# Kernel optimization log

Measured on AMD Instinct MI355X. Metric: run time of the kernel, lower is better.

## Reference

```python
import jax, jax.numpy as jnp
import numpy as np

N = 100000      # nodes
E = 1600000     # edges (avg degree 16)
F_IN = 128      # num_features
H = 64          # num_hidden
C = 40          # num_classes


def setup_inputs() -> dict:
    key = jax.random.key(0)
    ks = jax.random.split(key, 12)
    glorot = lambda k, fi, fo: jax.random.normal(k, (fi, fo), jnp.float32) * np.float32(1.0 / np.sqrt(fi))
    return {
        "x": jax.random.normal(ks[0], (N, F_IN), jnp.float32),
        "edge_index": jax.random.randint(ks[1], (2, E), 0, N, jnp.int64),
        "conv0_w": glorot(ks[2], F_IN, H), "conv0_b": jnp.zeros((H,), jnp.float32),
        "lin0_w": glorot(ks[3], H, H),     "lin0_b": jnp.zeros((H,), jnp.float32),
        "conv1_w": glorot(ks[4], H, H),    "conv1_b": jnp.zeros((H,), jnp.float32),
        "lin1_w": glorot(ks[5], H, H),     "lin1_b": jnp.zeros((H,), jnp.float32),
        "out_w": glorot(ks[6], 2 * H, C),  "out_b": jnp.zeros((C,), jnp.float32),
    }


def _gcn_conv(h, W, b, src, dst, norm, n):
    # h: [N, din] -> transform then symmetric-normalized scatter-add aggregation
    m = (h @ W)[src] * norm[:, None]           # [E+N, dout] gathered messages
    return jax.ops.segment_sum(m, dst, num_segments=n) + b


def reference(x, edge_index, conv0_w, conv0_b, lin0_w, lin0_b,
              conv1_w, conv1_b, lin1_w, lin1_b, out_w, out_b):
    n = x.shape[0]
    loops = jnp.arange(n, dtype=edge_index.dtype)
    src = jnp.concatenate([edge_index[0], loops])  # self-loops appended (GCNConv default)
    dst = jnp.concatenate([edge_index[1], loops])
    deg = jax.ops.segment_sum(jnp.ones_like(dst, x.dtype), dst, num_segments=n)
    dinv = jnp.where(deg > 0, jax.lax.rsqrt(deg), 0.0)
    norm = dinv[src] * dinv[dst]                   # D^-1/2 A D^-1/2 edge weights

    # layer 0 (dropout omitted: eval mode for deterministic reference)
    h = jax.nn.elu(_gcn_conv(x, conv0_w, conv0_b, src, dst, norm, n))
    y0 = h @ lin0_w + lin0_b
    # layer 1
    h = jax.nn.elu(_gcn_conv(h, conv1_w, conv1_b, src, dst, norm, n))
    y1 = h @ lin1_w + lin1_b

    z = jnp.concatenate([y0, y1], axis=1)          # [N, 2H] jumping-knowledge concat
    return z @ out_w + out_b                       # [N, C]
```

## Files before the change

### kernel.cpp

```cpp
#include <hip/hip_runtime.h>

#define DEVFN __device__ __forceinline__

typedef __attribute__((ext_vector_type(8))) short short8;
typedef __attribute__((ext_vector_type(4))) float float4v;

DEVFN float bf2f(unsigned short u) {
    union { unsigned int i; float f; } c;
    c.i = ((unsigned int)u) << 16;
    return c.f;
}

DEVFN unsigned short f2bf(float f) {
    union { float f; unsigned int i; } c;
    c.f = f;
    unsigned int u = c.i;
    return (unsigned short)((u + 0x7FFFu + ((u >> 16) & 1u)) >> 16);
}

DEVFN void addu4(float* acc, uint4 u) {
    unsigned int w[4] = {u.x, u.y, u.z, u.w};
#pragma unroll
    for (int k = 0; k < 4; k++) {
        union { unsigned int i; float f; } lo, hi;
        lo.i = w[k] << 16;
        hi.i = w[k] & 0xFFFF0000u;
        acc[2 * k]     += lo.f;
        acc[2 * k + 1] += hi.f;
    }
}


#define CHUNK 4096

__global__ __launch_bounds__(256) void k_count(const int* __restrict__ dst,
                                               int* __restrict__ Cmat, int E) {
    __shared__ int lh[1024];
    int t = threadIdx.x;
    for (int b = t; b < 1024; b += 256) lh[b] = 0;
    __syncthreads();
    int i0 = blockIdx.x * CHUNK;
    int i1 = i0 + CHUNK; if (i1 > E) i1 = E;
    for (int i = i0 + t; i < i1; i += 256) atomicAdd(&lh[dst[i] >> 8], 1);
    __syncthreads();
    int* row = Cmat + (size_t)blockIdx.x * 1024;
    for (int b = t; b < 1024; b += 256) row[b] = lh[b];
}

__global__ __launch_bounds__(256) void k_wscan(const int* __restrict__ Cmat,
                                               int* __restrict__ Omat,
                                               int* __restrict__ btot, int gC) {
    int b = (blockIdx.x * 256 + threadIdx.x) >> 6;
    int lane = threadIdx.x & 63;
    int base = 0;
    for (int c0 = 0; c0 < gC; c0 += 64) {
        int c = c0 + lane;
        int x = (c < gC) ? Cmat[(size_t)c * 1024 + b] : 0;
        int orig = x;
#pragma unroll
        for (int off = 1; off < 64; off <<= 1) {
            int y = __shfl_up(x, off);
            if (lane >= off) x += y;
        }
        if (c < gC) Omat[(size_t)c * 1024 + b] = base + x - orig;
        base += __shfl(x, 63);
    }
    if (lane == 0) btot[b] = base;
}

__global__ __launch_bounds__(1024) void k_bscan(const int* __restrict__ btot,
                                                int* __restrict__ boff) {
    __shared__ int s[1024];
    int t = threadIdx.x;
    int v = btot[t];
    s[t] = v;
    __syncthreads();
    for (int o = 1; o < 1024; o <<= 1) {
        int x = (t >= o) ? s[t - o] : 0;
        __syncthreads();
        s[t] += x;
        __syncthreads();
    }
    boff[t] = s[t] - v;
    if (t == 1023) boff[1024] = s[t];
}

__global__ __launch_bounds__(256) void k_part2(const int* __restrict__ src,
                                               const int* __restrict__ dst,
                                               const int* __restrict__ Omat,
                                               const int* __restrict__ boff,
                                               unsigned int* __restrict__ part, int E) {
    __shared__ int lb[1024];
    __shared__ int lc[1024];
    int t = threadIdx.x;
    const int* orow = Omat + (size_t)blockIdx.x * 1024;
    for (int b = t; b < 1024; b += 256) {
        lb[b] = boff[b] + orow[b];
        lc[b] = 0;
    }
    __syncthreads();
    int i0 = blockIdx.x * CHUNK;
    int i1 = i0 + CHUNK; if (i1 > E) i1 = E;
    for (int i = i0 + t; i < i1; i += 256) {
        int d = dst[i];
        int b = d >> 8;
        int r = atomicAdd(&lc[b], 1);
        part[lb[b] + r] = (unsigned int)src[i] | ((unsigned int)(d & 255) << 24);
    }
}

__global__ __launch_bounds__(256) void k_fill_local(const unsigned int* __restrict__ part,
                                                    const int* __restrict__ boff,
                                                    float* __restrict__ dinv,
                                                    int* __restrict__ roff,
                                                    int* __restrict__ csr, int n) {
    __shared__ int lcnt[256];
    __shared__ int lsc[256];
    __shared__ int lcur[256];
    int b = blockIdx.x, t = threadIdx.x;
    int s0 = boff[b], s1 = boff[b + 1];
    lcnt[t] = 0;
    __syncthreads();
    for (int i = s0 + t; i < s1; i += 256) atomicAdd(&lcnt[part[i] >> 24], 1);
    __syncthreads();
    int v = lcnt[t];
    lsc[t] = v;
    __syncthreads();
    for (int o = 1; o < 256; o <<= 1) {
        int x = (t >= o) ? lsc[t - o] : 0;
        __syncthreads();
        lsc[t] += x;
        __syncthreads();
    }
    int excl = lsc[t] - v;
    int node = (b << 8) + t;
    if (node < n) {
        dinv[node] = rsqrtf((float)(v + 1));
        roff[node] = s0 + excl + v;
    }
    lcur[t] = s0 + excl;
    __syncthreads();
    for (int i = s0 + t; i < s1; i += 256) {
        unsigned int p = part[i];
        int pos = atomicAdd(&lcur[p >> 24], 1);
        csr[pos] = (int)(p & 0xFFFFFFu);
    }
}

__global__ __launch_bounds__(256) void k_prep(const float* __restrict__ W0,
                                              const float* __restrict__ W1,
                                              const float* __restrict__ lin0_w, const float* __restrict__ lin0_b,
                                              const float* __restrict__ lin1_w, const float* __restrict__ lin1_b,
                                              const float* __restrict__ out_w, const float* __restrict__ out_b,
                                              unsigned short* __restrict__ Wb0,
                                              unsigned short* __restrict__ Wb1,
                                              unsigned short* __restrict__ Wfb0,
                                              float* __restrict__ Wf1p,
                                              float* __restrict__ bfv) {
    int tid = blockIdx.x * 256 + threadIdx.x;
    if (tid < 1024) {
        int ks = tid >> 8, rem = tid & 255;
        int nt = rem >> 6, lane = rem & 63;
        int quad = lane >> 4, c = lane & 15;
        union { unsigned short h[8]; uint4 u; } p;
#pragma unroll
        for (int j = 0; j < 8; j++)
            p.h[j] = f2bf(W0[(ks * 32 + quad * 8 + j) * 64 + nt * 16 + c]);
        *(uint4*)(Wb0 + (size_t)tid * 8) = p.u;
    } else if (tid < 1536) {
        int t2 = tid - 1024;
        int ks = t2 >> 8, rem = t2 & 255;
        int nt = rem >> 6, lane = rem & 63;
        int quad = lane >> 4, c = lane & 15;
        union { unsigned short h[8]; uint4 u; } p;
#pragma unroll
        for (int j = 0; j < 8; j++)
            p.h[j] = f2bf(W1[(ks * 32 + quad * 8 + j) * 64 + nt * 16 + c]);
        *(uint4*)(Wb1 + (size_t)t2 * 8) = p.u;
    } else if (tid < 1920) {
        int t2 = tid - 1536;
        int ks = t2 / 192;
        int rem = t2 % 192;
        int nt = rem >> 6, lane = rem & 63;
        int quad = lane >> 4, c = lane & 15;
        int col = nt * 16 + c;
        union { unsigned short h[8]; uint4 u; } p;
#pragma unroll
        for (int j = 0; j < 8; j++) {
            unsigned short r = 0;
            if (col < 40) {
                int i = ks * 32 + quad * 8 + j;
                float a = 0.f;
                for (int k = 0; k < 64; k++) a += lin0_w[i * 64 + k] * out_w[k * 40 + col];
                r = f2bf(a);
            }
            p.h[j] = r;
        }
        *(uint4*)(Wfb0 + ((size_t)(ks * 3 + nt) * 64 + lane) * 8) = p.u;
    } else if (tid < 1960) {
        int j = tid - 1920;
        float a = out_b[j];
        for (int k = 0; k < 64; k++) {
            a += lin0_b[k] * out_w[k * 40 + j];
            a += lin1_b[k] * out_w[(64 + k) * 40 + j];
        }
        bfv[j] = a;
    } else if (tid < 4520) {
        int t2 = tid - 1960;
        int i = t2 / 40, c = t2 % 40;
        float a = 0.f;
        for (int k = 0; k < 64; k++) a += lin1_w[i * 64 + k] * out_w[(64 + k) * 40 + c];
        Wf1p[i * 40 + c] = a;
    }
}


__global__ __launch_bounds__(256) void k_gemm_128(const float* __restrict__ A,
                                                  const unsigned short* __restrict__ Wb,
                                                  const float* __restrict__ dinv,
                                                  unsigned short* __restrict__ Cb, int n) {
    __shared__ unsigned short aLDS[64 * 144];
    int t = threadIdx.x;
    int r0 = blockIdx.x * 64;
    for (int idx = t; idx < 2048; idx += 256) {
        int r = idx >> 5;
        int k = (idx & 31) << 2;
        int gr = r0 + r; if (gr >= n) gr = n - 1;
        float4 u = *(const float4*)(A + (size_t)gr * 128 + k);
        int tile = r >> 4, m = r & 15;
        int ks = k >> 5, quad = (k >> 3) & 3, j0 = k & 7;
        int g = (tile * 4 + ks) * 4 + quad;
        union { unsigned short h[4]; uint2 u2; } pk;
        pk.h[0] = f2bf(u.x); pk.h[1] = f2bf(u.y); pk.h[2] = f2bf(u.z); pk.h[3] = f2bf(u.w);
        *(uint2*)(aLDS + g * 144 + m * 8 + j0) = pk.u2;
    }
    int lane = t & 63;
    int w = t >> 6;
    short8 bfr[4][4];
#pragma unroll
    for (int ks = 0; ks < 4; ks++)
#pragma unroll
        for (int nt = 0; nt < 4; nt++)
            bfr[ks][nt] = *(const short8*)(Wb + ((size_t)(ks * 4 + nt) * 64 + lane) * 8);
    __syncthreads();
    int quad = lane >> 4, m = lane & 15;
    short8 afr[4];
#pragma unroll
    for (int ks = 0; ks < 4; ks++)
        afr[ks] = *(const short8*)(aLDS + ((w * 4 + ks) * 4 + quad) * 144 + m * 8);
    float4v acc[4] = {};
#pragma unroll
    for (int nt = 0; nt < 4; nt++)
#pragma unroll
        for (int ks = 0; ks < 4; ks++)
            acc[nt] = __builtin_amdgcn_mfma_f32_16x16x32_bf16(afr[ks], bfr[ks][nt], acc[nt], 0, 0, 0);
    float dv[4];
#pragma unroll
    for (int reg = 0; reg < 4; reg++) {
        int gr = r0 + w * 16 + quad * 4 + reg;
        dv[reg] = (gr < n) ? dinv[gr] : 0.f;
    }
#pragma unroll
    for (int nt = 0; nt < 4; nt++)
#pragma unroll
        for (int reg = 0; reg < 4; reg++) {
            int gr = r0 + w * 16 + quad * 4 + reg;
            if (gr < n) Cb[(size_t)gr * 64 + nt * 16 + m] = f2bf(dv[reg] * acc[nt][reg]);
        }
}

__global__ __launch_bounds__(256) void k_mid(const unsigned short* __restrict__ Hb,
                                             const unsigned short* __restrict__ Wb,
                                             const unsigned short* __restrict__ Wfb,
                                             const float* __restrict__ dinv,
                                             unsigned short* __restrict__ Ab,
                                             float* __restrict__ O, int n) {
    __shared__ unsigned short aLDS[32 * 144];
    int t = threadIdx.x;
    int r0 = blockIdx.x * 64;
    for (int idx = t; idx < 512; idx += 256) {
        int r = idx >> 3, j = idx & 7;
        int gr = r0 + r; if (gr >= n) gr = n - 1;
        uint4 u = *(const uint4*)(Hb + (size_t)gr * 64 + j * 8);
        int tile = r >> 4, m = r & 15;
        int ks = j >> 2, quad = j & 3;
        *(uint4*)(aLDS + ((tile * 2 + ks) * 4 + quad) * 144 + m * 8) = u;
    }
    int lane = t & 63;
    int w = t >> 6;
    short8 bG[2][4], bH[2][3];
#pragma unroll
    for (int ks = 0; ks < 2; ks++) {
#pragma unroll
        for (int nt = 0; nt < 4; nt++)
            bG[ks][nt] = *(const short8*)(Wb + ((size_t)(ks * 4 + nt) * 64 + lane) * 8);
#pragma unroll
        for (int nt = 0; nt < 3; nt++)
            bH[ks][nt] = *(const short8*)(Wfb + ((size_t)(ks * 3 + nt) * 64 + lane) * 8);
    }
    __syncthreads();
    int quad = lane >> 4, m = lane & 15;
    short8 afr[2];
#pragma unroll
    for (int ks = 0; ks < 2; ks++)
        afr[ks] = *(const short8*)(aLDS + ((w * 2 + ks) * 4 + quad) * 144 + m * 8);
    float4v accG[4] = {};
    float4v accH[3] = {};
#pragma unroll
    for (int nt = 0; nt < 4; nt++)
#pragma unroll
        for (int ks = 0; ks < 2; ks++)
            accG[nt] = __builtin_amdgcn_mfma_f32_16x16x32_bf16(afr[ks], bG[ks][nt], accG[nt], 0, 0, 0);
#pragma unroll
    for (int nt = 0; nt < 3; nt++)
#pragma unroll
        for (int ks = 0; ks < 2; ks++)
            accH[nt] = __builtin_amdgcn_mfma_f32_16x16x32_bf16(afr[ks], bH[ks][nt], accH[nt], 0, 0, 0);
    float dv[4];
#pragma unroll
    for (int reg = 0; reg < 4; reg++) {
        int gr = r0 + w * 16 + quad * 4 + reg;
        dv[reg] = (gr < n) ? dinv[gr] : 0.f;
    }
#pragma unroll
    for (int nt = 0; nt < 4; nt++)
#pragma unroll
        for (int reg = 0; reg < 4; reg++) {
            int gr = r0 + w * 16 + quad * 4 + reg;
            if (gr < n) Ab[(size_t)gr * 64 + nt * 16 + m] = f2bf(dv[reg] * accG[nt][reg]);
        }
#pragma unroll
    for (int nt = 0; nt < 3; nt++) {
        int col = nt * 16 + m;
        if (col < 40) {
#pragma unroll
            for (int reg = 0; reg < 4; reg++) {
                int gr = r0 + w * 16 + quad * 4 + reg;
                if (gr < n) O[(size_t)gr * 40 + col] = accH[nt][reg];
            }
        }
    }
}

__global__ __launch_bounds__(256) void k_agg(const unsigned short* __restrict__ T,
                                             const int* __restrict__ csr,
                                             const int* __restrict__ roffE,
                                             const float* __restrict__ bias,
                                             unsigned short* __restrict__ Hb, int n) {
    int lane = threadIdx.x & 63;
    int half = lane >> 5;
    int sub = lane & 31;
    int q = sub >> 3, h = sub & 7;
    int hb = half << 5;
    int v = blockIdx.x * 8 + ((threadIdx.x >> 6) << 1) + half;
    if (v >= n) return;
    int start = (v == 0) ? 0 : roffE[v - 1];
    int end = roffE[v];
    float dv = rsqrtf((float)(end - start + 1));
    float acc[8] = {0.f, 0.f, 0.f, 0.f, 0.f, 0.f, 0.f, 0.f};
    if (q == 0) {
        uint4 u = *(const uint4*)(T + (size_t)v * 64 + h * 8);
        addu4(acc, u);
    }
    for (int base = start; base < end; base += 32) {
        int m = end - base; if (m > 32) m = 32;
        int e = (sub < m) ? csr[base + sub] : 0;
        int j = 0;
        for (; j + 16 <= m; j += 16) {
            int s0 = __shfl(e, hb + j + q);
            int s1 = __shfl(e, hb + j + 4 + q);
            int s2 = __shfl(e, hb + j + 8 + q);
            int s3 = __shfl(e, hb + j + 12 + q);
            uint4 u0 = *(const uint4*)(T + (size_t)s0 * 64 + h * 8);
            uint4 u1 = *(const uint4*)(T + (size_t)s1 * 64 + h * 8);
            uint4 u2 = *(const uint4*)(T + (size_t)s2 * 64 + h * 8);
            uint4 u3 = *(const uint4*)(T + (size_t)s3 * 64 + h * 8);
            addu4(acc, u0); addu4(acc, u1); addu4(acc, u2); addu4(acc, u3);
        }
        if (j + 8 <= m) {
            int s0 = __shfl(e, hb + j + q);
            int s1 = __shfl(e, hb + j + 4 + q);
            uint4 u0 = *(const uint4*)(T + (size_t)s0 * 64 + h * 8);
            uint4 u1 = *(const uint4*)(T + (size_t)s1 * 64 + h * 8);
            addu4(acc, u0); addu4(acc, u1);
            j += 8;
        }
        if (j + 4 <= m) {
            int s = __shfl(e, hb + j + q);
            uint4 u = *(const uint4*)(T + (size_t)s * 64 + h * 8);
            addu4(acc, u);
            j += 4;
        }
        if (j < m) {
            int jj = j + q;
            int s = __shfl(e, hb + (jj & 31));
            if (jj < m) {
                uint4 u = *(const uint4*)(T + (size_t)s * 64 + h * 8);
                addu4(acc, u);
            }
        }
    }
#pragma unroll
    for (int i = 0; i < 8; i++) {
        acc[i] += __shfl_xor(acc[i], 8);
        acc[i] += __shfl_xor(acc[i], 16);
    }
    if (q == 0) {
        float4 b0 = *(const float4*)(bias + h * 8);
        float4 b1 = *(const float4*)(bias + h * 8 + 4);
        float bb[8] = {b0.x, b0.y, b0.z, b0.w, b1.x, b1.y, b1.z, b1.w};
        union { unsigned short hh[8]; uint4 u; } p;
#pragma unroll
        for (int i = 0; i < 8; i++) {
            float r = dv * acc[i] + bb[i];
            r = (r > 0.f) ? r : (__expf(r) - 1.f);
            p.hh[i] = f2bf(r);
        }
        *(uint4*)(Hb + (size_t)v * 64 + h * 8) = p.u;
    }
}

__global__ __launch_bounds__(256) void k_agg_head(const unsigned short* __restrict__ T,
                                                  const int* __restrict__ csr,
                                                  const int* __restrict__ roffE,
                                                  const float* __restrict__ bias,
                                                  const float* __restrict__ Wf1p,
                                                  const float* __restrict__ bfv,
                                                  float* __restrict__ O, int n) {
    __shared__ float Ws[64 * 41];
    int t = threadIdx.x;
    for (int idx = t; idx < 2560; idx += 256) {
        int k = idx / 40, c = idx % 40;
        Ws[k * 41 + c] = Wf1p[idx];
    }
    __syncthreads();
    int lane = t & 63;
    int half = lane >> 5;
    int sub = lane & 31;
    int q = sub >> 3, h = sub & 7;
    int hb = half << 5;
    int v = blockIdx.x * 8 + ((t >> 6) << 1) + half;
    if (v >= n) return;
    int start = (v == 0) ? 0 : roffE[v - 1];
    int end = roffE[v];
    float dv = rsqrtf((float)(end - start + 1));
    float acc[8] = {0.f, 0.f, 0.f, 0.f, 0.f, 0.f, 0.f, 0.f};
    if (q == 0) {
        uint4 u = *(const uint4*)(T + (size_t)v * 64 + h * 8);
        addu4(acc, u);
    }
    for (int base = start; base < end; base += 32) {
        int m = end - base; if (m > 32) m = 32;
        int e = (sub < m) ? csr[base + sub] : 0;
        int j = 0;
        for (; j + 16 <= m; j += 16) {
            int s0 = __shfl(e, hb + j + q);
            int s1 = __shfl(e, hb + j + 4 + q);
            int s2 = __shfl(e, hb + j + 8 + q);
            int s3 = __shfl(e, hb + j + 12 + q);
            uint4 u0 = *(const uint4*)(T + (size_t)s0 * 64 + h * 8);
            uint4 u1 = *(const uint4*)(T + (size_t)s1 * 64 + h * 8);
            uint4 u2 = *(const uint4*)(T + (size_t)s2 * 64 + h * 8);
            uint4 u3 = *(const uint4*)(T + (size_t)s3 * 64 + h * 8);
            addu4(acc, u0); addu4(acc, u1); addu4(acc, u2); addu4(acc, u3);
        }
        if (j + 8 <= m) {
            int s0 = __shfl(e, hb + j + q);
            int s1 = __shfl(e, hb + j + 4 + q);
            uint4 u0 = *(const uint4*)(T + (size_t)s0 * 64 + h * 8);
            uint4 u1 = *(const uint4*)(T + (size_t)s1 * 64 + h * 8);
            addu4(acc, u0); addu4(acc, u1);
            j += 8;
        }
        if (j + 4 <= m) {
            int s = __shfl(e, hb + j + q);
            uint4 u = *(const uint4*)(T + (size_t)s * 64 + h * 8);
            addu4(acc, u);
            j += 4;
        }
        if (j < m) {
            int jj = j + q;
            int s = __shfl(e, hb + (jj & 31));
            if (jj < m) {
                uint4 u = *(const uint4*)(T + (size_t)s * 64 + h * 8);
                addu4(acc, u);
            }
        }
    }
#pragma unroll
    for (int i = 0; i < 8; i++) {
        acc[i] += __shfl_xor(acc[i], 8);
        acc[i] += __shfl_xor(acc[i], 16);
    }
    float4 b0 = *(const float4*)(bias + h * 8);
    float4 b1 = *(const float4*)(bias + h * 8 + 4);
    float bb[8] = {b0.x, b0.y, b0.z, b0.w, b1.x, b1.y, b1.z, b1.w};
    float r[8];
#pragma unroll
    for (int i = 0; i < 8; i++) {
        float x = dv * acc[i] + bb[i];
        r[i] = (x > 0.f) ? x : (__expf(x) - 1.f);
    }
    const float* wrow = Ws + (h * 8) * 41 + q * 10;
    float p[10];
#pragma unroll
    for (int j = 0; j < 10; j++) {
        float s = 0.f;
#pragma unroll
        for (int i = 0; i < 8; i++) s += r[i] * wrow[i * 41 + j];
        p[j] = s;
    }
#pragma unroll
    for (int j = 0; j < 10; j++) {
        p[j] += __shfl_xor(p[j], 1);
        p[j] += __shfl_xor(p[j], 2);
        p[j] += __shfl_xor(p[j], 4);
    }
    int c0 = q * 10;
    size_t ob = (size_t)v * 40 + c0;
#pragma unroll
    for (int j = 0; j < 8; j++)
        if (h == j) O[ob + j] += p[j] + bfv[c0 + j];
    if (h == 0) O[ob + 8] += p[8] + bfv[c0 + 8];
    if (h == 1) O[ob + 9] += p[9] + bfv[c0 + 9];
}


extern "C" void kernel_launch(void* const* d_in, const int* in_sizes, int n_in,
                              void* d_out, int out_size, void* d_ws, size_t ws_size,
                              hipStream_t stream) {
    const float* x       = (const float*)d_in[0];
    const int*   eidx    = (const int*)d_in[1];
    const float* conv0_w = (const float*)d_in[2];
    const float* conv0_b = (const float*)d_in[3];
    const float* lin0_w  = (const float*)d_in[4];
    const float* lin0_b  = (const float*)d_in[5];
    const float* conv1_w = (const float*)d_in[6];
    const float* conv1_b = (const float*)d_in[7];
    const float* lin1_w  = (const float*)d_in[8];
    const float* lin1_b  = (const float*)d_in[9];
    const float* out_w   = (const float*)d_in[10];
    const float* out_b   = (const float*)d_in[11];

    int n = in_sizes[0] / 128;
    int E = in_sizes[1] / 2;
    const int* src = eidx;
    const int* dst = eidx + E;
    int NB = (n + 255) >> 8;
    int gC = (E + CHUNK - 1) / CHUNK;

    char* wsb = (char*)d_ws;
    auto al = [](size_t v) { return (v + 4095) & ~(size_t)4095; };
    size_t o = 0;
    int*            Cmat  = (int*)(wsb + o);            o = al(o + (size_t)gC * 1024 * 4);
    int*            Omat  = (int*)(wsb + o);            o = al(o + (size_t)gC * 1024 * 4);
    int*            btot  = (int*)(wsb + o);            o = al(o + 1024 * 4);
    int*            boff  = (int*)(wsb + o);            o = al(o + 1025 * 4);
    float*          dinv  = (float*)(wsb + o);          o = al(o + (size_t)n * 4);
    int*            roff  = (int*)(wsb + o);            o = al(o + (size_t)n * 4);
    unsigned int*   part  = (unsigned int*)(wsb + o);   o = al(o + (size_t)E * 4);
    int*            csr   = (int*)(wsb + o);            o = al(o + (size_t)E * 4);
    float*          bfv   = (float*)(wsb + o);          o = al(o + 40 * 4);
    unsigned short* Wb0   = (unsigned short*)(wsb + o); o = al(o + 8192 * 2);
    unsigned short* Wb1   = (unsigned short*)(wsb + o); o = al(o + 4096 * 2);
    unsigned short* Wfb0  = (unsigned short*)(wsb + o); o = al(o + 3072 * 2);
    float*          Wf1p  = (float*)(wsb + o);          o = al(o + 2560 * 4);
    unsigned short* Ab    = (unsigned short*)(wsb + o); o = al(o + (size_t)n * 64 * 2);
    unsigned short* Hb    = (unsigned short*)(wsb + o); o = al(o + (size_t)n * 64 * 2);
    float* O = (float*)d_out;

    int gT = (n + 63) / 64;
    int gV = (n + 7) / 8;

    k_count<<<gC, 256, 0, stream>>>(dst, Cmat, E);
    k_wscan<<<256, 256, 0, stream>>>(Cmat, Omat, btot, gC);
    k_bscan<<<1, 1024, 0, stream>>>(btot, boff);
    k_part2<<<gC, 256, 0, stream>>>(src, dst, Omat, boff, part, E);
    k_fill_local<<<NB, 256, 0, stream>>>(part, boff, dinv, roff, csr, n);
    k_prep<<<18, 256, 0, stream>>>(conv0_w, conv1_w, lin0_w, lin0_b, lin1_w, lin1_b,
                                   out_w, out_b, Wb0, Wb1, Wfb0, Wf1p, bfv);

    k_gemm_128<<<gT, 256, 0, stream>>>(x, Wb0, dinv, Ab, n);
    k_agg<<<gV, 256, 0, stream>>>(Ab, csr, roff, conv0_b, Hb, n);
    k_mid<<<gT, 256, 0, stream>>>(Hb, Wb1, Wfb0, dinv, Ab, O, n);
    k_agg_head<<<gV, 256, 0, stream>>>(Ab, csr, roff, conv1_b, Wf1p, bfv, O, n);
}
```

Measured before the change: 302.2 us.

## Process two nodes per half-wave in aggregation and split head into MFMA kernel

The aggregation kernel now handles two destination nodes per 32-lane half-wave. For degrees up to 32 it issues all neighbor gathers up front, using a zero padding row at index n so padded lanes load valid memory. The fused second aggregation plus scalar head projection is replaced by the same aggregation kernel followed by a separate bf16 MFMA head kernel, with the lin1·out weight prepacked in bf16. This aims to raise memory-level parallelism in the gathers and move the head GEMM onto matrix cores. In exchange it adds an extra kernel launch, round-trips the hidden activations through memory, and rounds the head weight to bf16.

```diff
diff --git a/kernel.cpp b/kernel.cpp
--- a/kernel.cpp
+++ b/kernel.cpp
@@ -155,8 +155,9 @@
                                               unsigned short* __restrict__ Wb0,
                                               unsigned short* __restrict__ Wb1,
                                               unsigned short* __restrict__ Wfb0,
-                                              float* __restrict__ Wf1p,
-                                              float* __restrict__ bfv) {
+                                              unsigned short* __restrict__ Wfb1,
+                                              float* __restrict__ bfv,
+                                              unsigned short* __restrict__ Ab, int n) {
     int tid = blockIdx.x * 256 + threadIdx.x;
     if (tid < 1024) {
         int ks = tid >> 8, rem = tid & 255;
@@ -197,20 +198,37 @@
             p.h[j] = r;
         }
         *(uint4*)(Wfb0 + ((size_t)(ks * 3 + nt) * 64 + lane) * 8) = p.u;
-    } else if (tid < 1960) {
-        int j = tid - 1920;
+    } else if (tid < 2304) {
+        int t2 = tid - 1920;
+        int ks = t2 / 192;
+        int rem = t2 % 192;
+        int nt = rem >> 6, lane = rem & 63;
+        int quad = lane >> 4, c = lane & 15;
+        int col = nt * 16 + c;
+        union { unsigned short h[8]; uint4 u; } p;
+#pragma unroll
+        for (int j = 0; j < 8; j++) {
+            unsigned short r = 0;
+            if (col < 40) {
+                int i = ks * 32 + quad * 8 + j;
+                float a = 0.f;
+                for (int k = 0; k < 64; k++) a += lin1_w[i * 64 + k] * out_w[(64 + k) * 40 + col];
+                r = f2bf(a);
+            }
+            p.h[j] = r;
+        }
+        *(uint4*)(Wfb1 + ((size_t)(ks * 3 + nt) * 64 + lane) * 8) = p.u;
+    } else if (tid < 2344) {
+        int j = tid - 2304;
         float a = out_b[j];
         for (int k = 0; k < 64; k++) {
             a += lin0_b[k] * out_w[k * 40 + j];
             a += lin1_b[k] * out_w[(64 + k) * 40 + j];
         }
         bfv[j] = a;
-    } else if (tid < 4520) {
-        int t2 = tid - 1960;
-        int i = t2 / 40, c = t2 % 40;
-        float a = 0.f;
-        for (int k = 0; k < 64; k++) a += lin1_w[i * 64 + k] * out_w[(64 + k) * 40 + c];
-        Wf1p[i * 40 + c] = a;
+    } else if (tid < 2352) {
+        uint4 z = {0u, 0u, 0u, 0u};
+        *(uint4*)(Ab + (size_t)n * 64 + (tid - 2344) * 8) = z;
     }
 }
 
@@ -342,26 +360,60 @@
     }
 }
 
-__global__ __launch_bounds__(256) void k_agg(const unsigned short* __restrict__ T,
-                                             const int* __restrict__ csr,
-                                             const int* __restrict__ roffE,
-                                             const float* __restrict__ bias,
-                                             unsigned short* __restrict__ Hb, int n) {
-    int lane = threadIdx.x & 63;
-    int half = lane >> 5;
-    int sub = lane & 31;
-    int q = sub >> 3, h = sub & 7;
-    int hb = half << 5;
-    int v = blockIdx.x * 8 + ((threadIdx.x >> 6) << 1) + half;
-    if (v >= n) return;
-    int start = (v == 0) ? 0 : roffE[v - 1];
-    int end = roffE[v];
-    float dv = rsqrtf((float)(end - start + 1));
-    float acc[8] = {0.f, 0.f, 0.f, 0.f, 0.f, 0.f, 0.f, 0.f};
-    if (q == 0) {
-        uint4 u = *(const uint4*)(T + (size_t)v * 64 + h * 8);
-        addu4(acc, u);
-    }
+__global__ __launch_bounds__(256) void k_head(const unsigned short* __restrict__ Hb,
+                                              const unsigned short* __restrict__ Wfb,
+                                              const float* __restrict__ bfv,
+                                              float* __restrict__ O, int n) {
+    __shared__ unsigned short aLDS[32 * 144];
+    int t = threadIdx.x;
+    int r0 = blockIdx.x * 64;
+    for (int idx = t; idx < 512; idx += 256) {
+        int r = idx >> 3, j = idx & 7;
+        int gr = r0 + r; if (gr >= n) gr = n - 1;
+        uint4 u = *(const uint4*)(Hb + (size_t)gr * 64 + j * 8);
+        int tile = r >> 4, m = r & 15;
+        int ks = j >> 2, quad = j & 3;
+        *(uint4*)(aLDS + ((tile * 2 + ks) * 4 + quad) * 144 + m * 8) = u;
+    }
+    int lane = t & 63;
+    int w = t >> 6;
+    short8 bfr[2][3];
+#pragma unroll
+    for (int ks = 0; ks < 2; ks++)
+#pragma unroll
+        for (int nt = 0; nt < 3; nt++)
+            bfr[ks][nt] = *(const short8*)(Wfb + ((size_t)(ks * 3 + nt) * 64 + lane) * 8);
+    __syncthreads();
+    int quad = lane >> 4, m = lane & 15;
+    short8 afr[2];
+#pragma unroll
+    for (int ks = 0; ks < 2; ks++)
+        afr[ks] = *(const short8*)(aLDS + ((w * 2 + ks) * 4 + quad) * 144 + m * 8);
+    float4v acc[3] = {};
+#pragma unroll
+    for (int nt = 0; nt < 3; nt++)
+#pragma unroll
+        for (int ks = 0; ks < 2; ks++)
+            acc[nt] = __builtin_amdgcn_mfma_f32_16x16x32_bf16(afr[ks], bfr[ks][nt], acc[nt], 0, 0, 0);
+#pragma unroll
+    for (int nt = 0; nt < 3; nt++) {
+        int col = nt * 16 + m;
+        if (col < 40) {
+            float bb = bfv[col];
+#pragma unroll
+            for (int reg = 0; reg < 4; reg++) {
+                int gr = r0 + w * 16 + quad * 4 + reg;
+                if (gr < n) {
+                    size_t p = (size_t)gr * 40 + col;
+                    O[p] = O[p] + acc[nt][reg] + bb;
+                }
+            }
+        }
+    }
+}
+
+DEVFN void agg_loop(const unsigned short* __restrict__ T, const int* __restrict__ csr,
+                    int start, int end, int hb, int sub, int q, int h, float* acc) {
     for (int base = start; base < end; base += 32) {
         int m = end - base; if (m > 32) m = 32;
         int e = (sub < m) ? csr[base + sub] : 0;
@@ -400,129 +452,103 @@
             }
         }
     }
+}
+
+__global__ __launch_bounds__(256) void k_agg2(const unsigned short* __restrict__ T,
+                                              const int* __restrict__ csr,
+                                              const int* __restrict__ roffE,
+                                              const float* __restrict__ bias,
+                                              unsigned short* __restrict__ Hb, int n) {
+    int lane = threadIdx.x & 63;
+    int half = lane >> 5;
+    int sub = lane & 31;
+    int q = sub >> 3, h = sub & 7;
+    int hb = half << 5;
+    int w = threadIdx.x >> 6;
+    int v0 = blockIdx.x * 16 + w * 4 + half * 2;
+    if (v0 >= n) return;
+    int v1 = v0 + 1;
+    bool has1 = (v1 < n);
+    int sA = (v0 == 0) ? 0 : roffE[v0 - 1];
+    int eA = roffE[v0];
+    int eB = has1 ? roffE[v1] : eA;
+    int mA = eA - sA;
+    int mB = eB - eA;
+    float dvA = rsqrtf((float)(mA + 1));
+    float dvB = rsqrtf((float)(mB + 1));
+    float accA[8] = {0.f, 0.f, 0.f, 0.f, 0.f, 0.f, 0.f, 0.f};
+    float accB[8] = {0.f, 0.f, 0.f, 0.f, 0.f, 0.f, 0.f, 0.f};
+    uint4 uSA = {0u, 0u, 0u, 0u}, uSB = {0u, 0u, 0u, 0u};
+    if (q == 0) {
+        uSA = *(const uint4*)(T + (size_t)v0 * 64 + h * 8);
+        if (has1) uSB = *(const uint4*)(T + (size_t)v1 * 64 + h * 8);
+    }
+    if (mA <= 32 && mB <= 32) {
+        int e0 = (sub < mA) ? csr[sA + sub] : n;
+        int e1 = (sub < mB) ? csr[eA + sub] : n;
+        int a0 = __shfl(e0, hb + q),      a1 = __shfl(e0, hb + 4 + q);
+        int a2 = __shfl(e0, hb + 8 + q),  a3 = __shfl(e0, hb + 12 + q);
+        int b0 = __shfl(e1, hb + q),      b1 = __shfl(e1, hb + 4 + q);
+        int b2 = __shfl(e1, hb + 8 + q),  b3 = __shfl(e1, hb + 12 + q);
+        uint4 uA0 = *(const uint4*)(T + (size_t)a0 * 64 + h * 8);
+        uint4 uA1 = *(const uint4*)(T + (size_t)a1 * 64 + h * 8);
+        uint4 uA2 = *(const uint4*)(T + (size_t)a2 * 64 + h * 8);
+        uint4 uA3 = *(const uint4*)(T + (size_t)a3 * 64 + h * 8);
+        uint4 uB0 = *(const uint4*)(T + (size_t)b0 * 64 + h * 8);
+        uint4 uB1 = *(const uint4*)(T + (size_t)b1 * 64 + h * 8);
+        uint4 uB2 = *(const uint4*)(T + (size_t)b2 * 64 + h * 8);
+        uint4 uB3 = *(const uint4*)(T + (size_t)b3 * 64 + h * 8);
+        bool tA = (mA > 16), tB = (mB > 16);
+        if (tA) {
+            int a4 = __shfl(e0, hb + 16 + q), a5 = __shfl(e0, hb + 20 + q);
+            int a6 = __shfl(e0, hb + 24 + q), a7 = __shfl(e0, hb + 28 + q);
+            uint4 u4 = *(const uint4*)(T + (size_t)a4 * 64 + h * 8);
+            uint4 u5 = *(const uint4*)(T + (size_t)a5 * 64 + h * 8);
+            uint4 u6 = *(const uint4*)(T + (size_t)a6 * 64 + h * 8);
+            uint4 u7 = *(const uint4*)(T + (size_t)a7 * 64 + h * 8);
+            addu4(accA, u4); addu4(accA, u5); addu4(accA, u6); addu4(accA, u7);
+        }
+        if (tB) {
+            int b4 = __shfl(e1, hb + 16 + q), b5 = __shfl(e1, hb + 20 + q);
+            int b6 = __shfl(e1, hb + 24 + q), b7 = __shfl(e1, hb + 28 + q);
+            uint4 u4 = *(const uint4*)(T + (size_t)b4 * 64 + h * 8);
+            uint4 u5 = *(const uint4*)(T + (size_t)b5 * 64 + h * 8);
+            uint4 u6 = *(const uint4*)(T + (size_t)b6 * 64 + h * 8);
+            uint4 u7 = *(const uint4*)(T + (size_t)b7 * 64 + h * 8);
+            addu4(accB, u4); addu4(accB, u5); addu4(accB, u6); addu4(accB, u7);
+        }
+        addu4(accA, uA0); addu4(accA, uA1); addu4(accA, uA2); addu4(accA, uA3);
+        addu4(accB, uB0); addu4(accB, uB1); addu4(accB, uB2); addu4(accB, uB3);
+    } else {
+        agg_loop(T, csr, sA, eA, hb, sub, q, h, accA);
+        agg_loop(T, csr, eA, eB, hb, sub, q, h, accB);
+    }
+    addu4(accA, uSA);
+    addu4(accB, uSB);
 #pragma unroll
     for (int i = 0; i < 8; i++) {
-        acc[i] += __shfl_xor(acc[i], 8);
-        acc[i] += __shfl_xor(acc[i], 16);
+        accA[i] += __shfl_xor(accA[i], 8);
+        accA[i] += __shfl_xor(accA[i], 16);
+        accB[i] += __shfl_xor(accB[i], 8);
+        accB[i] += __shfl_xor(accB[i], 16);
     }
     if (q == 0) {
         float4 b0 = *(const float4*)(bias + h * 8);
         float4 b1 = *(const float4*)(bias + h * 8 + 4);
         float bb[8] = {b0.x, b0.y, b0.z, b0.w, b1.x, b1.y, b1.z, b1.w};
-        union { unsigned short hh[8]; uint4 u; } p;
+        union { unsigned short hh[8]; uint4 u; } pA, pB;
 #pragma unroll
         for (int i = 0; i < 8; i++) {
-            float r = dv * acc[i] + bb[i];
-            r = (r > 0.f) ? r : (__expf(r) - 1.f);
-            p.hh[i] = f2bf(r);
-        }
-        *(uint4*)(Hb + (size_t)v * 64 + h * 8) = p.u;
-    }
-}
-
-__global__ __launch_bounds__(256) void k_agg_head(const unsigned short* __restrict__ T,
-                                                  const int* __restrict__ csr,
-                                                  const int* __restrict__ roffE,
-                                                  const float* __restrict__ bias,
-                                                  const float* __restrict__ Wf1p,
-                                                  const float* __restrict__ bfv,
-                                                  float* __restrict__ O, int n) {
-    __shared__ float Ws[64 * 41];
-    int t = threadIdx.x;
-    for (int idx = t; idx < 2560; idx += 256) {
-        int k = idx / 40, c = idx % 40;
-        Ws[k * 41 + c] = Wf1p[idx];
-    }
-    __syncthreads();
-    int lane = t & 63;
-    int half = lane >> 5;
-    int sub = lane & 31;
-    int q = sub >> 3, h = sub & 7;
-    int hb = half << 5;
-    int v = blockIdx.x * 8 + ((t >> 6) << 1) + half;
-    if (v >= n) return;
-    int start = (v == 0) ? 0 : roffE[v - 1];
-    int end = roffE[v];
-    float dv = rsqrtf((float)(end - start + 1));
-    float acc[8] = {0.f, 0.f, 0.f, 0.f, 0.f, 0.f, 0.f, 0.f};
-    if (q == 0) {
-        uint4 u = *(const uint4*)(T + (size_t)v * 64 + h * 8);
-        addu4(acc, u);
-    }
-    for (int base = start; base < end; base += 32) {
-        int m = end - base; if (m > 32) m = 32;
-        int e = (sub < m) ? csr[base + sub] : 0;
-        int j = 0;
-        for (; j + 16 <= m; j += 16) {
-            int s0 = __shfl(e, hb + j + q);
-            int s1 = __shfl(e, hb + j + 4 + q);
-            int s2 = __shfl(e, hb + j + 8 + q);
-            int s3 = __shfl(e, hb + j + 12 + q);
-            uint4 u0 = *(const uint4*)(T + (size_t)s0 * 64 + h * 8);
-            uint4 u1 = *(const uint4*)(T + (size_t)s1 * 64 + h * 8);
-            uint4 u2 = *(const uint4*)(T + (size_t)s2 * 64 + h * 8);
-            uint4 u3 = *(const uint4*)(T + (size_t)s3 * 64 + h * 8);
-            addu4(acc, u0); addu4(acc, u1); addu4(acc, u2); addu4(acc, u3);
-        }
-        if (j + 8 <= m) {
-            int s0 = __shfl(e, hb + j + q);
-            int s1 = __shfl(e, hb + j + 4 + q);
-            uint4 u0 = *(const uint4*)(T + (size_t)s0 * 64 + h * 8);
-            uint4 u1 = *(const uint4*)(T + (size_t)s1 * 64 + h * 8);
-            addu4(acc, u0); addu4(acc, u1);
-            j += 8;
-        }
-        if (j + 4 <= m) {
-            int s = __shfl(e, hb + j + q);
-            uint4 u = *(const uint4*)(T + (size_t)s * 64 + h * 8);
-            addu4(acc, u);
-            j += 4;
-        }
-        if (j < m) {
-            int jj = j + q;
-            int s = __shfl(e, hb + (jj & 31));
-            if (jj < m) {
-                uint4 u = *(const uint4*)(T + (size_t)s * 64 + h * 8);
-                addu4(acc, u);
-            }
-        }
-    }
-#pragma unroll
-    for (int i = 0; i < 8; i++) {
-        acc[i] += __shfl_xor(acc[i], 8);
-        acc[i] += __shfl_xor(acc[i], 16);
-    }
-    float4 b0 = *(const float4*)(bias + h * 8);
-    float4 b1 = *(const float4*)(bias + h * 8 + 4);
-    float bb[8] = {b0.x, b0.y, b0.z, b0.w, b1.x, b1.y, b1.z, b1.w};
-    float r[8];
-#pragma unroll
-    for (int i = 0; i < 8; i++) {
-        float x = dv * acc[i] + bb[i];
-        r[i] = (x > 0.f) ? x : (__expf(x) - 1.f);
-    }
-    const float* wrow = Ws + (h * 8) * 41 + q * 10;
-    float p[10];
-#pragma unroll
-    for (int j = 0; j < 10; j++) {
-        float s = 0.f;
-#pragma unroll
-        for (int i = 0; i < 8; i++) s += r[i] * wrow[i * 41 + j];
-        p[j] = s;
-    }
-#pragma unroll
-    for (int j = 0; j < 10; j++) {
-        p[j] += __shfl_xor(p[j], 1);
-        p[j] += __shfl_xor(p[j], 2);
-        p[j] += __shfl_xor(p[j], 4);
-    }
-    int c0 = q * 10;
-    size_t ob = (size_t)v * 40 + c0;
-#pragma unroll
-    for (int j = 0; j < 8; j++)
-        if (h == j) O[ob + j] += p[j] + bfv[c0 + j];
-    if (h == 0) O[ob + 8] += p[8] + bfv[c0 + 8];
-    if (h == 1) O[ob + 9] += p[9] + bfv[c0 + 9];
+            float rA = dvA * accA[i] + bb[i];
+            rA = (rA > 0.f) ? rA : (__expf(rA) - 1.f);
+            pA.hh[i] = f2bf(rA);
+            float rB = dvB * accB[i] + bb[i];
+            rB = (rB > 0.f) ? rB : (__expf(rB) - 1.f);
+            pB.hh[i] = f2bf(rB);
+        }
+        *(uint4*)(Hb + (size_t)v0 * 64 + h * 8) = pA.u;
+        if (has1) *(uint4*)(Hb + (size_t)v1 * 64 + h * 8) = pB.u;
+    }
 }
 
 
@@ -564,24 +590,25 @@
     unsigned short* Wb0   = (unsigned short*)(wsb + o); o = al(o + 8192 * 2);
     unsigned short* Wb1   = (unsigned short*)(wsb + o); o = al(o + 4096 * 2);
     unsigned short* Wfb0  = (unsigned short*)(wsb + o); o = al(o + 3072 * 2);
-    float*          Wf1p  = (float*)(wsb + o);          o = al(o + 2560 * 4);
-    unsigned short* Ab    = (unsigned short*)(wsb + o); o = al(o + (size_t)n * 64 * 2);
+    unsigned short* Wfb1  = (unsigned short*)(wsb + o); o = al(o + 3072 * 2);
+    unsigned short* Ab    = (unsigned short*)(wsb + o); o = al(o + (size_t)(n + 1) * 64 * 2);
     unsigned short* Hb    = (unsigned short*)(wsb + o); o = al(o + (size_t)n * 64 * 2);
     float* O = (float*)d_out;
 
     int gT = (n + 63) / 64;
-    int gV = (n + 7) / 8;
+    int gV2 = (n + 15) / 16;
 
     k_count<<<gC, 256, 0, stream>>>(dst, Cmat, E);
     k_wscan<<<256, 256, 0, stream>>>(Cmat, Omat, btot, gC);
     k_bscan<<<1, 1024, 0, stream>>>(btot, boff);
     k_part2<<<gC, 256, 0, stream>>>(src, dst, Omat, boff, part, E);
     k_fill_local<<<NB, 256, 0, stream>>>(part, boff, dinv, roff, csr, n);
-    k_prep<<<18, 256, 0, stream>>>(conv0_w, conv1_w, lin0_w, lin0_b, lin1_w, lin1_b,
-                                   out_w, out_b, Wb0, Wb1, Wfb0, Wf1p, bfv);
+    k_prep<<<10, 256, 0, stream>>>(conv0_w, conv1_w, lin0_w, lin0_b, lin1_w, lin1_b,
+                                   out_w, out_b, Wb0, Wb1, Wfb0, Wfb1, bfv, Ab, n);
 
     k_gemm_128<<<gT, 256, 0, stream>>>(x, Wb0, dinv, Ab, n);
-    k_agg<<<gV, 256, 0, stream>>>(Ab, csr, roff, conv0_b, Hb, n);
+    k_agg2<<<gV2, 256, 0, stream>>>(Ab, csr, roff, conv0_b, Hb, n);
     k_mid<<<gT, 256, 0, stream>>>(Hb, Wb1, Wfb0, dinv, Ab, O, n);
-    k_agg_head<<<gV, 256, 0, stream>>>(Ab, csr, roff, conv1_b, Wf1p, bfv, O, n);
-}
+    k_agg2<<<gV2, 256, 0, stream>>>(Ab, csr, roff, conv1_b, Hb, n);
+    k_head<<<gT, 256, 0, stream>>>(Hb, Wfb1, bfv, O, n);
+}
```

Measured after the change: 275.9 us. 1.1x faster.
